# Kernel tuning notes

Hardware: AMD Instinct MI355X
Metric: run time of the kernel (lower is better)

## Reference

```python
import jax, jax.numpy as jnp
import numpy as np

# --- obs layout constants (from source) ---
OBS_TERM_DIMS = (3, 3, 3, 3, 29, 29, 29, 96)
HISTORY_LEN = 5
BASE_LIN_VEL_DIM = 3
_OFFS = [0]
for d in OBS_TERM_DIMS[:-1]:
    _OFFS.append(_OFFS[-1] + d * HISTORY_LEN)

N = 131072

def _extract_frame(x, frame_idx):
    # proprio frame: 7 terms, 99 dims total
    parts = []
    for t in range(7):
        d = OBS_TERM_DIMS[t]
        s = _OFFS[t] + frame_idx * d
        parts.append(x[:, s:s + d])
    return jnp.concatenate(parts, axis=-1)

def _extract_elevation(x):
    s = _OFFS[7] + (HISTORY_LEN - 1) * OBS_TERM_DIMS[7]
    return x[:, s:s + OBS_TERM_DIMS[7]]  # [N,96]

def setup_inputs() -> dict:
    key = jax.random.key(0)
    ks = jax.random.split(key, 16)
    s = 0.05
    return {
        "x": jax.random.normal(ks[0], (N, 975), jnp.float32),
        "vae_W1": jax.random.normal(ks[1], (480, 256), jnp.float32) * s,
        "vae_b1": jnp.zeros((256,), jnp.float32),
        "vae_Wz": jax.random.normal(ks[2], (256, 32), jnp.float32) * s,
        "vae_bz": jnp.zeros((32,), jnp.float32),
        "vae_Wv": jax.random.normal(ks[3], (256, 3), jnp.float32) * s,
        "vae_bv": jnp.zeros((3,), jnp.float32),
        "ae_W1": jax.random.normal(ks[4], (96, 64), jnp.float32) * s,
        "ae_b1": jnp.zeros((64,), jnp.float32),
        "ae_W2": jax.random.normal(ks[5], (64, 32), jnp.float32) * s,
        "ae_b2": jnp.zeros((32,), jnp.float32),
        "gate_W1": jax.random.normal(ks[6], (32, 64), jnp.float32) * s,
        "gate_b1": jnp.zeros((64,), jnp.float32),
        "gate_W2": jax.random.normal(ks[7], (64, 5), jnp.float32) * s,
        "gate_b2": jnp.zeros((5,), jnp.float32),
        "eW1": jax.random.normal(ks[8], (5, 166, 128), jnp.float32) * s,
        "eb1": jnp.zeros((5, 128), jnp.float32),
        "eW2": jax.random.normal(ks[9], (5, 128, 128), jnp.float32) * s,
        "eb2": jnp.zeros((5, 128), jnp.float32),
        "eW3": jax.random.normal(ks[10], (5, 128, 29), jnp.float32) * s,
        "eb3": jnp.zeros((5, 29), jnp.float32),
    }

def reference(x, vae_W1, vae_b1, vae_Wz, vae_bz, vae_Wv, vae_bv,
              ae_W1, ae_b1, ae_W2, ae_b2,
              gate_W1, gate_b1, gate_W2, gate_b2,
              eW1, eb1, eW2, eb2, eW3, eb3):
    elu = jax.nn.elu
    # feature extraction
    o_t = _extract_frame(x, HISTORY_LEN - 1)                       # [N,99]
    frames = [_extract_frame(x, i)[:, BASE_LIN_VEL_DIM:] for i in range(HISTORY_LEN)]
    vae_hist = jnp.concatenate(frames, axis=-1)                    # [N,480]
    e_t = _extract_elevation(x)                                    # [N,96]
    # VAE estimator (no_grad in original)
    h = elu(vae_hist @ vae_W1 + vae_b1)
    z_H = jax.lax.stop_gradient(h @ vae_Wz + vae_bz)               # [N,32]
    v_pred = jax.lax.stop_gradient(h @ vae_Wv + vae_bv)            # [N,3]
    # AE estimator (no_grad)
    ha = elu(e_t @ ae_W1 + ae_b1)
    z_E = jax.lax.stop_gradient(ha @ ae_W2 + ae_b2)                # [N,32]
    # experts: batched GEMM over 5 experts
    inp = jnp.concatenate([o_t, v_pred, z_H, z_E], axis=-1)        # [N,166]
    h1 = elu(jnp.einsum('ni,eih->neh', inp, eW1) + eb1)            # [N,5,128]
    h2 = elu(jnp.einsum('neh,ehk->nek', h1, eW2) + eb2)            # [N,5,128]
    acts = jnp.einsum('neh,ehk->nek', h2, eW3) + eb3               # [N,5,29]
    # gating
    gl = elu(z_E @ gate_W1 + gate_b1) @ gate_W2 + gate_b2          # [N,5]
    w = jax.nn.softmax(gl, axis=-1)
    return jnp.einsum('ne,nek->nk', w, acts)                       # [N,29]
```

## Files before the change

kernel.cpp:

```cpp
#include <hip/hip_runtime.h>
#include <math.h>

typedef _Float16 f16;
typedef f16  f16x8 __attribute__((ext_vector_type(8)));
typedef float f32x4 __attribute__((ext_vector_type(4)));
typedef unsigned short ushort_t;

#define MFMA16(a, b, c) __builtin_amdgcn_mfma_f32_16x16x32_f16((a), (b), (c), 0, 0, 0)

#define W1T_E 0
#define WZV_E 122880
#define A1T_E 135168
#define A2T_E 141312
#define G1T_E 143360
#define G2T_E 145408
#define E1T_E 146432
#define E2T_E 269312
#define E3T_E 351232
#define F32_B 743424

#define B0_OFF  0
#define B1_OFF  25600
#define ET_OFF  38912
#define HA_OFF  52224
#define H_OFF   38912
#define H1_OFF  38912
#define H2_OFF  56320
#define W_OFF   73728
#define MAP_OFF 75776
#define SMEM_SZ 76160

__device__ __forceinline__ float elu_f(float v) {
    float e = __expf(v) - 1.f;
    return v > 0.f ? v : e;
}

__device__ __forceinline__ unsigned pk(float a, float b) {
    ushort_t u0 = __builtin_bit_cast(ushort_t, (f16)a);
    ushort_t u1 = __builtin_bit_cast(ushort_t, (f16)b);
    return (unsigned)u0 | ((unsigned)u1 << 16);
}

__device__ __forceinline__ void store4(f16* p, f32x4 v) {
    uint2 t; t.x = pk(v[0], v[1]); t.y = pk(v[2], v[3]);
    *(uint2*)p = t;
}

__device__ __forceinline__ void elu_store4(f16* p, f32x4 v) {
    uint2 t; t.x = pk(elu_f(v[0]), elu_f(v[1])); t.y = pk(elu_f(v[2]), elu_f(v[3]));
    *(uint2*)p = t;
}

__global__ void prep_kernel(const float* __restrict__ vW1, const float* __restrict__ vWz,
                            const float* __restrict__ vWv, const float* __restrict__ aW1,
                            const float* __restrict__ aW2, const float* __restrict__ gW1,
                            const float* __restrict__ gW2, const float* __restrict__ eW1,
                            const float* __restrict__ eW2, const float* __restrict__ eW3,
                            const float* __restrict__ vbz, const float* __restrict__ vbv,
                            const float* __restrict__ eb3, const float* __restrict__ gb2,
                            char* __restrict__ ws)
{
    int i = blockIdx.x * 256 + threadIdx.x;
    f16* H = (f16*)ws;
    if (i < 122880) {
        int c = i / 480, k = i - c * 480;
        H[i] = (f16)vW1[k * 256 + c];
    } else if (i < 135168) {
        int j = i - 122880; int c = j / 256, k = j - c * 256;
        float v = (c < 32) ? vWz[k * 32 + c] : ((c < 35) ? vWv[k * 3 + (c - 32)] : 0.f);
        H[i] = (f16)v;
    } else if (i < 141312) {
        int j = i - 135168; int c = j / 96, k = j - c * 96;
        H[i] = (f16)aW1[k * 64 + c];
    } else if (i < 143360) {
        int j = i - 141312; int c = j / 64, k = j - c * 64;
        H[i] = (f16)aW2[k * 32 + c];
    } else if (i < 145408) {
        int j = i - 143360; int c = j / 32, k = j - c * 32;
        H[i] = (f16)gW1[k * 64 + c];
    } else if (i < 146432) {
        int j = i - 145408; int c = j / 64, k = j - c * 64;
        H[i] = (f16)((c < 5) ? gW2[k * 5 + c] : 0.f);
    } else if (i < 269312) {
        int j = i - 146432; int e = j / 24576, jj = j - e * 24576;
        int c = jj / 192, k = jj - c * 192;
        int ko = (k >= 5 && k < 107)   ? (k - 5)
               : (k >= 108 && k < 140) ? (k - 6)
               : (k >= 144 && k < 176) ? (k - 10) : -1;
        H[i] = (f16)((ko >= 0) ? eW1[(e * 166 + ko) * 128 + c] : 0.f);
    } else if (i < 351232) {
        int j = i - 269312; int e = j / 16384, jj = j - e * 16384;
        int c = jj / 128, k = jj - c * 128;
        H[i] = (f16)eW2[(e * 128 + k) * 128 + c];
    } else if (i < 371712) {
        int j = i - 351232; int e = j / 4096, jj = j - e * 4096;
        int c = jj / 128, k = jj - c * 128;
        H[i] = (f16)((c < 29) ? eW3[(e * 128 + k) * 29 + c] : 0.f);
    } else if (i < 371936) {
        int j = i - 371712;
        float* F = (float*)(ws + F32_B);
        float v;
        if (j < 48)       v = (j < 32) ? vbz[j] : ((j < 35) ? vbv[j - 32] : 0.f);
        else if (j < 208) { int t = j - 48; int e = t >> 5, c = t & 31;
                            v = (c < 29) ? eb3[e * 29 + c] : 0.f; }
        else              { int t = j - 208; v = (t < 5) ? gb2[t] : 0.f; }
        F[j] = v;
    }
}

__global__ __launch_bounds__(256, 2) void moe_fused(
    const float* __restrict__ x,
    const float* __restrict__ vb1,
    const float* __restrict__ ab1,
    const float* __restrict__ ab2,
    const float* __restrict__ gb1,
    const float* __restrict__ eb1,
    const float* __restrict__ eb2,
    const char* __restrict__ ws,
    float* __restrict__ out)
{
    __shared__ __align__(16) char smem[SMEM_SZ];
    const int tid  = threadIdx.x;
    const int wv   = tid >> 6;
    const int lane = tid & 63;
    const int lr   = lane & 15;
    const int lg   = lane >> 4;
    const int row0 = (int)blockIdx.x * 64;

    const f16* W1T = (const f16*)ws + W1T_E;
    const f16* WZV = (const f16*)ws + WZV_E;
    const f16* A1T = (const f16*)ws + A1T_E;
    const f16* A2T = (const f16*)ws + A2T_E;
    const f16* G1T = (const f16*)ws + G1T_E;
    const f16* G2T = (const f16*)ws + G2T_E;
    const f16* E1T = (const f16*)ws + E1T_E;
    const f16* E2T = (const f16*)ws + E2T_E;
    const f16* E3T = (const f16*)ws + E3T_E;
    const float* BZV  = (const float*)(ws + F32_B);
    const float* EB3P = BZV + 48;
    const float* GB2P = BZV + 208;

    f16* sB0 = (f16*)(smem + B0_OFF);
    f16* sB1 = (f16*)(smem + B1_OFF);
    f16* sEt = (f16*)(smem + ET_OFF);
    f16* sHA = (f16*)(smem + HA_OFF);
    f16* sH  = (f16*)(smem + H_OFF);
    f16* sH1 = (f16*)(smem + H1_OFF);
    f16* sH2 = (f16*)(smem + H2_OFF);
    float* sWf = (float*)(smem + W_OFF);
    unsigned* smap = (unsigned*)(smem + MAP_OFF);

    const char* xc = (const char*)x;
    const int srow = tid >> 2;
    const int cb   = 24 * (tid & 3);
    const bool lowc = ((tid & 3) == 0);

    if (tid < 96) {
        int c = tid; int base;
        if (c < 9)       { int t = c / 3; base = 15 + 12 * t + c; }
        else if (c < 38) base = 51 + c;
        else if (c < 67) base = 167 + c;
        else             base = 283 + c;
        smap[c] = (unsigned)(base * 4);
    }
    if (tid < 64) {
        f16* rp = sB0 + tid * 200;
        uint2 z2; z2.x = 0u; z2.y = 0u;
        *(uint2*)(rp + 0) = z2; rp[4] = (f16)0.f;
        *(uint2*)(rp + 140) = z2;
        uint4 z4; z4.x = z4.y = z4.z = z4.w = 0u;
        *(uint4*)(rp + 176) = z4; *(uint4*)(rp + 184) = z4;
    }
    if (tid < 192) {
        int r = tid / 3, c = tid - 3 * r;
        sB0[r * 200 + 5 + c] = (f16)x[(row0 + r) * 975 + 12 + c];
    }
    {
        const float* xr = x + (size_t)(row0 + srow) * 975 + 879 + cb;
        f16* dst = sEt + srow * 104 + cb;
#pragma unroll
        for (int k = 0; k < 24; k += 2) {
            *(unsigned*)(dst + k) = pk(xr[k], xr[k + 1]);
        }
    }
    __syncthreads();

    {
        f32x4 bi = *(const f32x4*)(ab1 + 16 * wv + 4 * lg);
        f32x4 acc[4];
#pragma unroll
        for (int m = 0; m < 4; ++m) acc[m] = bi;
#pragma unroll
        for (int ks = 0; ks < 3; ++ks) {
            f16x8 wf = *(const f16x8*)(A1T + (16 * wv + lr) * 96 + 32 * ks + 8 * lg);
#pragma unroll
            for (int m = 0; m < 4; ++m) {
                f16x8 bf = *(const f16x8*)(sEt + (16 * m + lr) * 104 + 32 * ks + 8 * lg);
                acc[m] = MFMA16(wf, bf, acc[m]);
            }
        }
#pragma unroll
        for (int m = 0; m < 4; ++m)
            elu_store4(sHA + (16 * m + lr) * 72 + 16 * wv + 4 * lg, acc[m]);
    }
    unsigned a_off[24];
    {
        unsigned rowb = (unsigned)(row0 + srow) * 3900u;
#pragma unroll
        for (int i = 0; i < 24; ++i) a_off[i] = rowb + smap[cb + i];
    }
    __syncthreads();

    if (wv < 2) {
        f32x4 bi = *(const f32x4*)(ab2 + 16 * wv + 4 * lg);
        f32x4 acc[4];
#pragma unroll
        for (int m = 0; m < 4; ++m) acc[m] = bi;
#pragma unroll
        for (int ks = 0; ks < 2; ++ks) {
            f16x8 wf = *(const f16x8*)(A2T + (16 * wv + lr) * 64 + 32 * ks + 8 * lg);
#pragma unroll
            for (int m = 0; m < 4; ++m) {
                f16x8 bf = *(const f16x8*)(sHA + (16 * m + lr) * 72 + 32 * ks + 8 * lg);
                acc[m] = MFMA16(wf, bf, acc[m]);
            }
        }
#pragma unroll
        for (int m = 0; m < 4; ++m)
            store4(sB0 + (16 * m + lr) * 200 + 144 + 16 * wv + 4 * lg, acc[m]);
    }
    {
        float tv[24];
#pragma unroll
        for (int i = 0; i < 24; ++i) tv[i] = *(const float*)(xc + a_off[i]);
        f16* dst = sB0 + srow * 200 + 8 + cb;
#pragma unroll
        for (int k = 0; k < 12; ++k) *(unsigned*)(dst + 2 * k) = pk(tv[2 * k], tv[2 * k + 1]);
#pragma unroll
        for (int i = 0; i < 24; ++i) a_off[i] += (lowc && i < 9) ? 12u : 116u;
    }
    __syncthreads();

    {
        f32x4 bi = *(const f32x4*)(gb1 + 16 * wv + 4 * lg);
        f32x4 acc[4];
#pragma unroll
        for (int m = 0; m < 4; ++m) acc[m] = bi;
        f16x8 wf = *(const f16x8*)(G1T + (16 * wv + lr) * 32 + 8 * lg);
#pragma unroll
        for (int m = 0; m < 4; ++m) {
            f16x8 bf = *(const f16x8*)(sB0 + (16 * m + lr) * 200 + 144 + 8 * lg);
            acc[m] = MFMA16(wf, bf, acc[m]);
        }
#pragma unroll
        for (int m = 0; m < 4; ++m)
            elu_store4(sHA + (16 * m + lr) * 72 + 16 * wv + 4 * lg, acc[m]);
    }
    __syncthreads();

    if (wv == 0) {
        f32x4 bi = *(const f32x4*)(GB2P + 4 * lg);
        f32x4 acc[4];
#pragma unroll
        for (int m = 0; m < 4; ++m) acc[m] = bi;
#pragma unroll
        for (int ks = 0; ks < 2; ++ks) {
            f16x8 wf = *(const f16x8*)(G2T + lr * 64 + 32 * ks + 8 * lg);
#pragma unroll
            for (int m = 0; m < 4; ++m) {
                f16x8 bf = *(const f16x8*)(sHA + (16 * m + lr) * 72 + 32 * ks + 8 * lg);
                acc[m] = MFMA16(wf, bf, acc[m]);
            }
        }
        if (lg == 0) {
#pragma unroll
            for (int m = 0; m < 4; ++m)
                *(f32x4*)(sWf + (16 * m + lr) * 8) = acc[m];
        } else if (lg == 1) {
#pragma unroll
            for (int m = 0; m < 4; ++m)
                sWf[(16 * m + lr) * 8 + 4] = acc[m][0];
        }
    }
    __syncthreads();

    f32x4 acc1[4][4];
#pragma unroll
    for (int nt = 0; nt < 4; ++nt) {
        f32x4 bi = *(const f32x4*)(vb1 + 64 * wv + 16 * nt + 4 * lg);
#pragma unroll
        for (int m = 0; m < 4; ++m) acc1[m][nt] = bi;
    }
    for (int f = 0; f < 5; ++f) {
        if (f == 0 && tid < 64) {
            float g[5];
#pragma unroll
            for (int e = 0; e < 5; ++e) g[e] = sWf[tid * 8 + e];
            float mx = fmaxf(fmaxf(fmaxf(g[0], g[1]), fmaxf(g[2], g[3])), g[4]);
            float s = 0.f;
#pragma unroll
            for (int e = 0; e < 5; ++e) { g[e] = __expf(g[e] - mx); s += g[e]; }
            float inv = 1.f / s;
#pragma unroll
            for (int e = 0; e < 5; ++e) sWf[tid * 8 + e] = g[e] * inv;
        }
        float tv[24];
        if (f < 4) {
#pragma unroll
            for (int i = 0; i < 24; ++i) tv[i] = *(const float*)(xc + a_off[i]);
        }
        const f16* Bp = (f & 1) ? sB1 : sB0;
        const int bst = (f & 1) ? 104 : 200;
#pragma unroll
        for (int ks = 0; ks < 3; ++ks) {
            f16x8 wf[4];
#pragma unroll
            for (int nt = 0; nt < 4; ++nt)
                wf[nt] = *(const f16x8*)(W1T + (64 * wv + 16 * nt + lr) * 480 + 96 * f + 32 * ks + 8 * lg);
#pragma unroll
            for (int m = 0; m < 4; ++m) {
                f16x8 bf = *(const f16x8*)(Bp + (16 * m + lr) * bst + 8 + 32 * ks + 8 * lg);
#pragma unroll
                for (int nt = 0; nt < 4; ++nt)
                    acc1[m][nt] = MFMA16(wf[nt], bf, acc1[m][nt]);
            }
        }
        if (f < 4) {
            f16* dst = (((f + 1) & 1) ? sB1 : sB0) + srow * (((f + 1) & 1) ? 104 : 200) + 8 + cb;
#pragma unroll
            for (int k = 0; k < 12; ++k) *(unsigned*)(dst + 2 * k) = pk(tv[2 * k], tv[2 * k + 1]);
#pragma unroll
            for (int i = 0; i < 24; ++i) a_off[i] += (lowc && i < 9) ? 12u : 116u;
        }
        if (f == 4) {
#pragma unroll
            for (int m = 0; m < 4; ++m)
#pragma unroll
                for (int nt = 0; nt < 4; ++nt)
                    elu_store4(sH + (16 * m + lr) * 264 + 64 * wv + 16 * nt + 4 * lg, acc1[m][nt]);
        }
        __syncthreads();
    }

    if (wv < 3) {
        f32x4 bz = *(const f32x4*)(BZV + 16 * wv + 4 * lg);
        f32x4 acc[4];
#pragma unroll
        for (int m = 0; m < 4; ++m) acc[m] = bz;
#pragma unroll
        for (int ks = 0; ks < 8; ++ks) {
            f16x8 wf = *(const f16x8*)(WZV + (16 * wv + lr) * 256 + 32 * ks + 8 * lg);
#pragma unroll
            for (int m = 0; m < 4; ++m) {
                f16x8 bf = *(const f16x8*)(sH + (16 * m + lr) * 264 + 32 * ks + 8 * lg);
                acc[m] = MFMA16(wf, bf, acc[m]);
            }
        }
        int j0 = 16 * wv + 4 * lg;
        if (wv < 2 || lg == 0) {
            int col = (wv < 2) ? (108 + j0) : 104;
#pragma unroll
            for (int m = 0; m < 4; ++m)
                store4(sB0 + (16 * m + lr) * 200 + col, acc[m]);
        }
    }
    __syncthreads();

    f32x4 oacc[2];
    oacc[0] = (f32x4)0.f; oacc[1] = (f32x4)0.f;

    for (int e = 0; e < 5; ++e) {
        {
            f32x4 acc[4][2];
#pragma unroll
            for (int nt = 0; nt < 2; ++nt) {
                f32x4 bi = *(const f32x4*)(eb1 + e * 128 + 32 * wv + 16 * nt + 4 * lg);
#pragma unroll
                for (int m = 0; m < 4; ++m) acc[m][nt] = bi;
            }
#pragma unroll
            for (int ks = 0; ks < 6; ++ks) {
                f16x8 wf[2];
#pragma unroll
                for (int nt = 0; nt < 2; ++nt)
                    wf[nt] = *(const f16x8*)(E1T + (e * 128 + 32 * wv + 16 * nt + lr) * 192 + 32 * ks + 8 * lg);
#pragma unroll
                for (int m = 0; m < 4; ++m) {
                    f16x8 bf = *(const f16x8*)(sB0 + (16 * m + lr) * 200 + 32 * ks + 8 * lg);
#pragma unroll
                    for (int nt = 0; nt < 2; ++nt) acc[m][nt] = MFMA16(wf[nt], bf, acc[m][nt]);
                }
            }
#pragma unroll
            for (int m = 0; m < 4; ++m)
#pragma unroll
                for (int nt = 0; nt < 2; ++nt)
                    elu_store4(sH1 + (16 * m + lr) * 136 + 32 * wv + 16 * nt + 4 * lg, acc[m][nt]);
        }
        __syncthreads();
        {
            f32x4 acc[4][2];
#pragma unroll
            for (int nt = 0; nt < 2; ++nt) {
                f32x4 bi = *(const f32x4*)(eb2 + e * 128 + 32 * wv + 16 * nt + 4 * lg);
#pragma unroll
                for (int m = 0; m < 4; ++m) acc[m][nt] = bi;
            }
#pragma unroll
            for (int ks = 0; ks < 4; ++ks) {
                f16x8 wf[2];
#pragma unroll
                for (int nt = 0; nt < 2; ++nt)
                    wf[nt] = *(const f16x8*)(E2T + (e * 128 + 32 * wv + 16 * nt + lr) * 128 + 32 * ks + 8 * lg);
#pragma unroll
                for (int m = 0; m < 4; ++m) {
                    f16x8 bf = *(const f16x8*)(sH1 + (16 * m + lr) * 136 + 32 * ks + 8 * lg);
#pragma unroll
                    for (int nt = 0; nt < 2; ++nt) acc[m][nt] = MFMA16(wf[nt], bf, acc[m][nt]);
                }
            }
#pragma unroll
            for (int m = 0; m < 4; ++m)
#pragma unroll
                for (int nt = 0; nt < 2; ++nt)
                    elu_store4(sH2 + (16 * m + lr) * 136 + 32 * wv + 16 * nt + 4 * lg, acc[m][nt]);
        }
        __syncthreads();
        {
            f32x4 acc3[2];
#pragma unroll
            for (int nt = 0; nt < 2; ++nt)
                acc3[nt] = *(const f32x4*)(EB3P + e * 32 + 16 * nt + 4 * lg);
#pragma unroll
            for (int ks = 0; ks < 4; ++ks) {
                f16x8 bf = *(const f16x8*)(sH2 + (16 * wv + lr) * 136 + 32 * ks + 8 * lg);
#pragma unroll
                for (int nt = 0; nt < 2; ++nt) {
                    f16x8 wf = *(const f16x8*)(E3T + (e * 32 + 16 * nt + lr) * 128 + 32 * ks + 8 * lg);
                    acc3[nt] = MFMA16(wf, bf, acc3[nt]);
                }
            }
            float we = sWf[(16 * wv + lr) * 8 + e];
#pragma unroll
            for (int nt = 0; nt < 2; ++nt)
#pragma unroll
                for (int r = 0; r < 4; ++r) oacc[nt][r] += we * acc3[nt][r];
        }
        __syncthreads();
    }

    {
        int row = row0 + 16 * wv + lr;
#pragma unroll
        for (int nt = 0; nt < 2; ++nt)
#pragma unroll
            for (int r = 0; r < 4; ++r) {
                int col = 16 * nt + 4 * lg + r;
                if (col < 29) out[row * 29 + col] = oacc[nt][r];
            }
    }
}

extern "C" void kernel_launch(void* const* d_in, const int* in_sizes, int n_in,
                              void* d_out, int out_size, void* d_ws, size_t ws_size,
                              hipStream_t stream)
{
    (void)n_in; (void)out_size; (void)ws_size;
    const float* x   = (const float*)d_in[0];
    const float* vW1 = (const float*)d_in[1];
    const float* vb1 = (const float*)d_in[2];
    const float* vWz = (const float*)d_in[3];
    const float* vbz = (const float*)d_in[4];
    const float* vWv = (const float*)d_in[5];
    const float* vbv = (const float*)d_in[6];
    const float* aW1 = (const float*)d_in[7];
    const float* ab1 = (const float*)d_in[8];
    const float* aW2 = (const float*)d_in[9];
    const float* ab2 = (const float*)d_in[10];
    const float* gW1 = (const float*)d_in[11];
    const float* gb1 = (const float*)d_in[12];
    const float* gW2 = (const float*)d_in[13];
    const float* gb2 = (const float*)d_in[14];
    const float* eW1 = (const float*)d_in[15];
    const float* eb1 = (const float*)d_in[16];
    const float* eW2 = (const float*)d_in[17];
    const float* eb2 = (const float*)d_in[18];
    const float* eW3 = (const float*)d_in[19];
    const float* eb3 = (const float*)d_in[20];

    int n = in_sizes[0] / 975;

    prep_kernel<<<(371936 + 255) / 256, 256, 0, stream>>>(
        vW1, vWz, vWv, aW1, aW2, gW1, gW2, eW1, eW2, eW3, vbz, vbv, eb3, gb2, (char*)d_ws);

    moe_fused<<<n / 64, 256, 0, stream>>>(
        x, vb1, ab1, ab2, gb1, eb1, eb2, (const char*)d_ws, (float*)d_out);
}
```

Baseline: 319.2 us.

## Shrink row tile to 48 and repack shared memory to fit three blocks per CU

Each block now handles 48 rows instead of 64, and the shared-memory staging buffers are overlapped so the footprint drops from about 76KB to about 47KB. Launch bounds are raised to three blocks per CU. Row loads are clamped and output stores masked so the tail block stays correct. The goal is more resident waves to hide memory and sync latency. The cost is that expert weights are reloaded per block across more blocks, MFMA reuse per weight fragment is lower, and one wave idles in the final layer.

```diff
diff --git a/kernel.cpp b/kernel.cpp
--- a/kernel.cpp
+++ b/kernel.cpp
@@ -20,15 +20,14 @@
 #define F32_B 743424
 
 #define B0_OFF  0
-#define B1_OFF  25600
-#define ET_OFF  38912
-#define HA_OFF  52224
-#define H_OFF   38912
-#define H1_OFF  38912
-#define H2_OFF  56320
-#define W_OFF   73728
-#define MAP_OFF 75776
-#define SMEM_SZ 76160
+#define SA_OFF  19200
+#define HA_OFF  29184
+#define H_OFF   19200
+#define H1_OFF  19200
+#define H2_OFF  32256
+#define W_OFF   45312
+#define MAP_OFF 46848
+#define SMEM_SZ 47232
 
 __device__ __forceinline__ float elu_f(float v) {
     float e = __expf(v) - 1.f;
@@ -108,7 +107,7 @@
     }
 }
 
-__global__ __launch_bounds__(256, 2) void moe_fused(
+__global__ __launch_bounds__(256, 3) void moe_fused(
     const float* __restrict__ x,
     const float* __restrict__ vb1,
     const float* __restrict__ ab1,
@@ -117,7 +116,8 @@
     const float* __restrict__ eb1,
     const float* __restrict__ eb2,
     const char* __restrict__ ws,
-    float* __restrict__ out)
+    float* __restrict__ out,
+    int n)
 {
     __shared__ __align__(16) char smem[SMEM_SZ];
     const int tid  = threadIdx.x;
@@ -125,7 +125,7 @@
     const int lane = tid & 63;
     const int lr   = lane & 15;
     const int lg   = lane >> 4;
-    const int row0 = (int)blockIdx.x * 64;
+    const int row0 = (int)blockIdx.x * 48;
 
     const f16* W1T = (const f16*)ws + W1T_E;
     const f16* WZV = (const f16*)ws + WZV_E;
@@ -141,8 +141,8 @@
     const float* GB2P = BZV + 208;
 
     f16* sB0 = (f16*)(smem + B0_OFF);
-    f16* sB1 = (f16*)(smem + B1_OFF);
-    f16* sEt = (f16*)(smem + ET_OFF);
+    f16* sB1 = (f16*)(smem + SA_OFF);
+    f16* sEt = (f16*)(smem + SA_OFF);
     f16* sHA = (f16*)(smem + HA_OFF);
     f16* sH  = (f16*)(smem + H_OFF);
     f16* sH1 = (f16*)(smem + H1_OFF);
@@ -154,6 +154,8 @@
     const int srow = tid >> 2;
     const int cb   = 24 * (tid & 3);
     const bool lowc = ((tid & 3) == 0);
+    const bool stg  = (tid < 192);
+    const int grow  = min(row0 + srow, n - 1);
 
     if (tid < 96) {
         int c = tid; int base;
@@ -163,7 +165,7 @@
         else             base = 283 + c;
         smap[c] = (unsigned)(base * 4);
     }
-    if (tid < 64) {
+    if (tid < 48) {
         f16* rp = sB0 + tid * 200;
         uint2 z2; z2.x = 0u; z2.y = 0u;
         *(uint2*)(rp + 0) = z2; rp[4] = (f16)0.f;
@@ -171,12 +173,13 @@
         uint4 z4; z4.x = z4.y = z4.z = z4.w = 0u;
         *(uint4*)(rp + 176) = z4; *(uint4*)(rp + 184) = z4;
     }
-    if (tid < 192) {
+    if (tid < 144) {
         int r = tid / 3, c = tid - 3 * r;
-        sB0[r * 200 + 5 + c] = (f16)x[(row0 + r) * 975 + 12 + c];
-    }
-    {
-        const float* xr = x + (size_t)(row0 + srow) * 975 + 879 + cb;
+        int gr = min(row0 + r, n - 1);
+        sB0[r * 200 + 5 + c] = (f16)x[(size_t)gr * 975 + 12 + c];
+    }
+    if (stg) {
+        const float* xr = x + (size_t)grow * 975 + 879 + cb;
         f16* dst = sEt + srow * 104 + cb;
 #pragma unroll
         for (int k = 0; k < 24; k += 2) {
@@ -187,25 +190,25 @@
 
     {
         f32x4 bi = *(const f32x4*)(ab1 + 16 * wv + 4 * lg);
-        f32x4 acc[4];
-#pragma unroll
-        for (int m = 0; m < 4; ++m) acc[m] = bi;
+        f32x4 acc[3];
+#pragma unroll
+        for (int m = 0; m < 3; ++m) acc[m] = bi;
 #pragma unroll
         for (int ks = 0; ks < 3; ++ks) {
             f16x8 wf = *(const f16x8*)(A1T + (16 * wv + lr) * 96 + 32 * ks + 8 * lg);
 #pragma unroll
-            for (int m = 0; m < 4; ++m) {
+            for (int m = 0; m < 3; ++m) {
                 f16x8 bf = *(const f16x8*)(sEt + (16 * m + lr) * 104 + 32 * ks + 8 * lg);
                 acc[m] = MFMA16(wf, bf, acc[m]);
             }
         }
 #pragma unroll
-        for (int m = 0; m < 4; ++m)
+        for (int m = 0; m < 3; ++m)
             elu_store4(sHA + (16 * m + lr) * 72 + 16 * wv + 4 * lg, acc[m]);
     }
     unsigned a_off[24];
     {
-        unsigned rowb = (unsigned)(row0 + srow) * 3900u;
+        unsigned rowb = (unsigned)grow * 3900u;
 #pragma unroll
         for (int i = 0; i < 24; ++i) a_off[i] = rowb + smap[cb + i];
     }
@@ -213,23 +216,23 @@
 
     if (wv < 2) {
         f32x4 bi = *(const f32x4*)(ab2 + 16 * wv + 4 * lg);
-        f32x4 acc[4];
-#pragma unroll
-        for (int m = 0; m < 4; ++m) acc[m] = bi;
+        f32x4 acc[3];
+#pragma unroll
+        for (int m = 0; m < 3; ++m) acc[m] = bi;
 #pragma unroll
         for (int ks = 0; ks < 2; ++ks) {
             f16x8 wf = *(const f16x8*)(A2T + (16 * wv + lr) * 64 + 32 * ks + 8 * lg);
 #pragma unroll
-            for (int m = 0; m < 4; ++m) {
+            for (int m = 0; m < 3; ++m) {
                 f16x8 bf = *(const f16x8*)(sHA + (16 * m + lr) * 72 + 32 * ks + 8 * lg);
                 acc[m] = MFMA16(wf, bf, acc[m]);
             }
         }
 #pragma unroll
-        for (int m = 0; m < 4; ++m)
+        for (int m = 0; m < 3; ++m)
             store4(sB0 + (16 * m + lr) * 200 + 144 + 16 * wv + 4 * lg, acc[m]);
     }
-    {
+    if (stg) {
         float tv[24];
 #pragma unroll
         for (int i = 0; i < 24; ++i) tv[i] = *(const float*)(xc + a_off[i]);
@@ -243,56 +246,56 @@
 
     {
         f32x4 bi = *(const f32x4*)(gb1 + 16 * wv + 4 * lg);
-        f32x4 acc[4];
-#pragma unroll
-        for (int m = 0; m < 4; ++m) acc[m] = bi;
+        f32x4 acc[3];
+#pragma unroll
+        for (int m = 0; m < 3; ++m) acc[m] = bi;
         f16x8 wf = *(const f16x8*)(G1T + (16 * wv + lr) * 32 + 8 * lg);
 #pragma unroll
-        for (int m = 0; m < 4; ++m) {
+        for (int m = 0; m < 3; ++m) {
             f16x8 bf = *(const f16x8*)(sB0 + (16 * m + lr) * 200 + 144 + 8 * lg);
             acc[m] = MFMA16(wf, bf, acc[m]);
         }
 #pragma unroll
-        for (int m = 0; m < 4; ++m)
+        for (int m = 0; m < 3; ++m)
             elu_store4(sHA + (16 * m + lr) * 72 + 16 * wv + 4 * lg, acc[m]);
     }
     __syncthreads();
 
     if (wv == 0) {
         f32x4 bi = *(const f32x4*)(GB2P + 4 * lg);
-        f32x4 acc[4];
-#pragma unroll
-        for (int m = 0; m < 4; ++m) acc[m] = bi;
+        f32x4 acc[3];
+#pragma unroll
+        for (int m = 0; m < 3; ++m) acc[m] = bi;
 #pragma unroll
         for (int ks = 0; ks < 2; ++ks) {
             f16x8 wf = *(const f16x8*)(G2T + lr * 64 + 32 * ks + 8 * lg);
 #pragma unroll
-            for (int m = 0; m < 4; ++m) {
+            for (int m = 0; m < 3; ++m) {
                 f16x8 bf = *(const f16x8*)(sHA + (16 * m + lr) * 72 + 32 * ks + 8 * lg);
                 acc[m] = MFMA16(wf, bf, acc[m]);
             }
         }
         if (lg == 0) {
 #pragma unroll
-            for (int m = 0; m < 4; ++m)
+            for (int m = 0; m < 3; ++m)
                 *(f32x4*)(sWf + (16 * m + lr) * 8) = acc[m];
         } else if (lg == 1) {
 #pragma unroll
-            for (int m = 0; m < 4; ++m)
+            for (int m = 0; m < 3; ++m)
                 sWf[(16 * m + lr) * 8 + 4] = acc[m][0];
         }
     }
     __syncthreads();
 
-    f32x4 acc1[4][4];
+    f32x4 acc1[3][4];
 #pragma unroll
     for (int nt = 0; nt < 4; ++nt) {
         f32x4 bi = *(const f32x4*)(vb1 + 64 * wv + 16 * nt + 4 * lg);
 #pragma unroll
-        for (int m = 0; m < 4; ++m) acc1[m][nt] = bi;
+        for (int m = 0; m < 3; ++m) acc1[m][nt] = bi;
     }
     for (int f = 0; f < 5; ++f) {
-        if (f == 0 && tid < 64) {
+        if (f == 0 && tid < 48) {
             float g[5];
 #pragma unroll
             for (int e = 0; e < 5; ++e) g[e] = sWf[tid * 8 + e];
@@ -305,7 +308,7 @@
             for (int e = 0; e < 5; ++e) sWf[tid * 8 + e] = g[e] * inv;
         }
         float tv[24];
-        if (f < 4) {
+        if (f < 4 && stg) {
 #pragma unroll
             for (int i = 0; i < 24; ++i) tv[i] = *(const float*)(xc + a_off[i]);
         }
@@ -318,14 +321,14 @@
             for (int nt = 0; nt < 4; ++nt)
                 wf[nt] = *(const f16x8*)(W1T + (64 * wv + 16 * nt + lr) * 480 + 96 * f + 32 * ks + 8 * lg);
 #pragma unroll
-            for (int m = 0; m < 4; ++m) {
+            for (int m = 0; m < 3; ++m) {
                 f16x8 bf = *(const f16x8*)(Bp + (16 * m + lr) * bst + 8 + 32 * ks + 8 * lg);
 #pragma unroll
                 for (int nt = 0; nt < 4; ++nt)
                     acc1[m][nt] = MFMA16(wf[nt], bf, acc1[m][nt]);
             }
         }
-        if (f < 4) {
+        if (f < 4 && stg) {
             f16* dst = (((f + 1) & 1) ? sB1 : sB0) + srow * (((f + 1) & 1) ? 104 : 200) + 8 + cb;
 #pragma unroll
             for (int k = 0; k < 12; ++k) *(unsigned*)(dst + 2 * k) = pk(tv[2 * k], tv[2 * k + 1]);
@@ -334,7 +337,7 @@
         }
         if (f == 4) {
 #pragma unroll
-            for (int m = 0; m < 4; ++m)
+            for (int m = 0; m < 3; ++m)
 #pragma unroll
                 for (int nt = 0; nt < 4; ++nt)
                     elu_store4(sH + (16 * m + lr) * 264 + 64 * wv + 16 * nt + 4 * lg, acc1[m][nt]);
@@ -344,14 +347,14 @@
 
     if (wv < 3) {
         f32x4 bz = *(const f32x4*)(BZV + 16 * wv + 4 * lg);
-        f32x4 acc[4];
-#pragma unroll
-        for (int m = 0; m < 4; ++m) acc[m] = bz;
+        f32x4 acc[3];
+#pragma unroll
+        for (int m = 0; m < 3; ++m) acc[m] = bz;
 #pragma unroll
         for (int ks = 0; ks < 8; ++ks) {
             f16x8 wf = *(const f16x8*)(WZV + (16 * wv + lr) * 256 + 32 * ks + 8 * lg);
 #pragma unroll
-            for (int m = 0; m < 4; ++m) {
+            for (int m = 0; m < 3; ++m) {
                 f16x8 bf = *(const f16x8*)(sH + (16 * m + lr) * 264 + 32 * ks + 8 * lg);
                 acc[m] = MFMA16(wf, bf, acc[m]);
             }
@@ -360,7 +363,7 @@
         if (wv < 2 || lg == 0) {
             int col = (wv < 2) ? (108 + j0) : 104;
 #pragma unroll
-            for (int m = 0; m < 4; ++m)
+            for (int m = 0; m < 3; ++m)
                 store4(sB0 + (16 * m + lr) * 200 + col, acc[m]);
         }
     }
@@ -371,12 +374,12 @@
 
     for (int e = 0; e < 5; ++e) {
         {
-            f32x4 acc[4][2];
+            f32x4 acc[3][2];
 #pragma unroll
             for (int nt = 0; nt < 2; ++nt) {
                 f32x4 bi = *(const f32x4*)(eb1 + e * 128 + 32 * wv + 16 * nt + 4 * lg);
 #pragma unroll
-                for (int m = 0; m < 4; ++m) acc[m][nt] = bi;
+                for (int m = 0; m < 3; ++m) acc[m][nt] = bi;
             }
 #pragma unroll
             for (int ks = 0; ks < 6; ++ks) {
@@ -385,26 +388,26 @@
                 for (int nt = 0; nt < 2; ++nt)
                     wf[nt] = *(const f16x8*)(E1T + (e * 128 + 32 * wv + 16 * nt + lr) * 192 + 32 * ks + 8 * lg);
 #pragma unroll
-                for (int m = 0; m < 4; ++m) {
+                for (int m = 0; m < 3; ++m) {
                     f16x8 bf = *(const f16x8*)(sB0 + (16 * m + lr) * 200 + 32 * ks + 8 * lg);
 #pragma unroll
                     for (int nt = 0; nt < 2; ++nt) acc[m][nt] = MFMA16(wf[nt], bf, acc[m][nt]);
                 }
             }
 #pragma unroll
-            for (int m = 0; m < 4; ++m)
+            for (int m = 0; m < 3; ++m)
 #pragma unroll
                 for (int nt = 0; nt < 2; ++nt)
                     elu_store4(sH1 + (16 * m + lr) * 136 + 32 * wv + 16 * nt + 4 * lg, acc[m][nt]);
         }
         __syncthreads();
         {
-            f32x4 acc[4][2];
+            f32x4 acc[3][2];
 #pragma unroll
             for (int nt = 0; nt < 2; ++nt) {
                 f32x4 bi = *(const f32x4*)(eb2 + e * 128 + 32 * wv + 16 * nt + 4 * lg);
 #pragma unroll
-                for (int m = 0; m < 4; ++m) acc[m][nt] = bi;
+                for (int m = 0; m < 3; ++m) acc[m][nt] = bi;
             }
 #pragma unroll
             for (int ks = 0; ks < 4; ++ks) {
@@ -413,20 +416,20 @@
                 for (int nt = 0; nt < 2; ++nt)
                     wf[nt] = *(const f16x8*)(E2T + (e * 128 + 32 * wv + 16 * nt + lr) * 128 + 32 * ks + 8 * lg);
 #pragma unroll
-                for (int m = 0; m < 4; ++m) {
+                for (int m = 0; m < 3; ++m) {
                     f16x8 bf = *(const f16x8*)(sH1 + (16 * m + lr) * 136 + 32 * ks + 8 * lg);
 #pragma unroll
                     for (int nt = 0; nt < 2; ++nt) acc[m][nt] = MFMA16(wf[nt], bf, acc[m][nt]);
                 }
             }
 #pragma unroll
-            for (int m = 0; m < 4; ++m)
+            for (int m = 0; m < 3; ++m)
 #pragma unroll
                 for (int nt = 0; nt < 2; ++nt)
                     elu_store4(sH2 + (16 * m + lr) * 136 + 32 * wv + 16 * nt + 4 * lg, acc[m][nt]);
         }
         __syncthreads();
-        {
+        if (wv < 3) {
             f32x4 acc3[2];
 #pragma unroll
             for (int nt = 0; nt < 2; ++nt)
@@ -449,15 +452,17 @@
         __syncthreads();
     }
 
-    {
+    if (wv < 3) {
         int row = row0 + 16 * wv + lr;
-#pragma unroll
-        for (int nt = 0; nt < 2; ++nt)
-#pragma unroll
-            for (int r = 0; r < 4; ++r) {
-                int col = 16 * nt + 4 * lg + r;
-                if (col < 29) out[row * 29 + col] = oacc[nt][r];
-            }
+        if (row < n) {
+#pragma unroll
+            for (int nt = 0; nt < 2; ++nt)
+#pragma unroll
+                for (int r = 0; r < 4; ++r) {
+                    int col = 16 * nt + 4 * lg + r;
+                    if (col < 29) out[(size_t)row * 29 + col] = oacc[nt][r];
+                }
+        }
     }
 }
 
@@ -493,6 +498,6 @@
     prep_kernel<<<(371936 + 255) / 256, 256, 0, stream>>>(
         vW1, vWz, vWv, aW1, aW2, gW1, gW2, eW1, eW2, eW3, vbz, vbv, eb3, gb2, (char*)d_ws);
 
-    moe_fused<<<n / 64, 256, 0, stream>>>(
-        x, vb1, ab1, ab2, gb1, eb1, eb2, (const char*)d_ws, (float*)d_out);
-}
+    moe_fused<<<(n + 47) / 48, 256, 0, stream>>>(
+        x, vb1, ab1, ab2, gb1, eb1, eb2, (const char*)d_ws, (float*)d_out, n);
+}
```

After: 348.0 us. 1.09x slower.

## Stage contiguous x slice in LDS and fold history gather into padded W1

Applied to the files above, without the earlier changes.

Instead of gathering the 480 scattered VAE history columns from x with per-thread offset tables across five pipelined frames, each block now copies the contiguous x columns 12..495 into shared memory with coalesced loads. The gather is moved into the prep kernel, which scatters vW1 rows into a 512-wide padded K layout, so the first GEMM runs as one 16-step K loop over the staged slice. The o_t features are then picked from that same staged buffer. This trades the reduced number of scattered global loads for about 6% extra MFMA work on the padded K, a larger shared-memory footprint, and a row-at-a-time staging loop per wave that has no double buffering.

```diff
diff --git a/kernel.cpp b/kernel.cpp
--- a/kernel.cpp
+++ b/kernel.cpp
@@ -9,26 +9,24 @@
 #define MFMA16(a, b, c) __builtin_amdgcn_mfma_f32_16x16x32_f16((a), (b), (c), 0, 0, 0)
 
 #define W1T_E 0
-#define WZV_E 122880
-#define A1T_E 135168
-#define A2T_E 141312
-#define G1T_E 143360
-#define G2T_E 145408
-#define E1T_E 146432
-#define E2T_E 269312
-#define E3T_E 351232
-#define F32_B 743424
-
-#define B0_OFF  0
-#define B1_OFF  25600
-#define ET_OFF  38912
-#define HA_OFF  52224
-#define H_OFF   38912
-#define H1_OFF  38912
-#define H2_OFF  56320
-#define W_OFF   73728
-#define MAP_OFF 75776
-#define SMEM_SZ 76160
+#define WZV_E 131072
+#define A1T_E 143360
+#define A2T_E 149504
+#define G1T_E 151552
+#define G2T_E 153600
+#define E1T_E 154624
+#define E2T_E 277504
+#define E3T_E 359424
+#define F32_B 759808
+
+#define S2_OFF   0
+#define B0_OFF   36864
+#define H2_OFF   17408
+#define ELEV_OFF 62528
+#define HA_OFF   62528
+#define ZE_OFF   71744
+#define WF_OFF   75840
+#define SMEM_SZ  77888
 
 __device__ __forceinline__ float elu_f(float v) {
     float e = __expf(v) - 1.f;
@@ -62,42 +60,55 @@
 {
     int i = blockIdx.x * 256 + threadIdx.x;
     f16* H = (f16*)ws;
-    if (i < 122880) {
-        int c = i / 480, k = i - c * 480;
-        H[i] = (f16)vW1[k * 256 + c];
-    } else if (i < 135168) {
-        int j = i - 122880; int c = j / 256, k = j - c * 256;
+    if (i < 131072) {
+        int c = i >> 9, ks = i & 511;
+        int xcol = 12 + ks;
+        float v = 0.f;
+        if (xcol >= 15 && xcol <= 494) {
+            int hc;
+            if (xcol < 60) {
+                int t = xcol / 15; int rm = xcol - 15 * t; int f = rm / 3;
+                hc = 96 * f + 3 * (t - 1) + (rm - 3 * f);
+            } else {
+                int t2 = (xcol - 60) / 145; int rm = xcol - 60 - 145 * t2; int f = rm / 29;
+                hc = 96 * f + 9 + 29 * t2 + (rm - 29 * f);
+            }
+            v = vW1[hc * 256 + c];
+        }
+        H[i] = (f16)v;
+    } else if (i < 143360) {
+        int j = i - 131072; int c = j / 256, k = j - c * 256;
         float v = (c < 32) ? vWz[k * 32 + c] : ((c < 35) ? vWv[k * 3 + (c - 32)] : 0.f);
         H[i] = (f16)v;
-    } else if (i < 141312) {
-        int j = i - 135168; int c = j / 96, k = j - c * 96;
+    } else if (i < 149504) {
+        int j = i - 143360; int c = j / 96, k = j - c * 96;
         H[i] = (f16)aW1[k * 64 + c];
-    } else if (i < 143360) {
-        int j = i - 141312; int c = j / 64, k = j - c * 64;
+    } else if (i < 151552) {
+        int j = i - 149504; int c = j / 64, k = j - c * 64;
         H[i] = (f16)aW2[k * 32 + c];
-    } else if (i < 145408) {
-        int j = i - 143360; int c = j / 32, k = j - c * 32;
+    } else if (i < 153600) {
+        int j = i - 151552; int c = j / 32, k = j - c * 32;
         H[i] = (f16)gW1[k * 64 + c];
-    } else if (i < 146432) {
-        int j = i - 145408; int c = j / 64, k = j - c * 64;
+    } else if (i < 154624) {
+        int j = i - 153600; int c = j / 64, k = j - c * 64;
         H[i] = (f16)((c < 5) ? gW2[k * 5 + c] : 0.f);
-    } else if (i < 269312) {
-        int j = i - 146432; int e = j / 24576, jj = j - e * 24576;
+    } else if (i < 277504) {
+        int j = i - 154624; int e = j / 24576, jj = j - e * 24576;
         int c = jj / 192, k = jj - c * 192;
         int ko = (k >= 5 && k < 107)   ? (k - 5)
                : (k >= 108 && k < 140) ? (k - 6)
                : (k >= 144 && k < 176) ? (k - 10) : -1;
         H[i] = (f16)((ko >= 0) ? eW1[(e * 166 + ko) * 128 + c] : 0.f);
-    } else if (i < 351232) {
-        int j = i - 269312; int e = j / 16384, jj = j - e * 16384;
+    } else if (i < 359424) {
+        int j = i - 277504; int e = j / 16384, jj = j - e * 16384;
         int c = jj / 128, k = jj - c * 128;
         H[i] = (f16)eW2[(e * 128 + k) * 128 + c];
-    } else if (i < 371712) {
-        int j = i - 351232; int e = j / 4096, jj = j - e * 4096;
+    } else if (i < 379904) {
+        int j = i - 359424; int e = j / 4096, jj = j - e * 4096;
         int c = jj / 128, k = jj - c * 128;
         H[i] = (f16)((c < 29) ? eW3[(e * 128 + k) * 29 + c] : 0.f);
-    } else if (i < 371936) {
-        int j = i - 371712;
+    } else if (i < 380128) {
+        int j = i - 379904;
         float* F = (float*)(ws + F32_B);
         float v;
         if (j < 48)       v = (j < 32) ? vbz[j] : ((j < 35) ? vbv[j - 32] : 0.f);
@@ -140,75 +151,59 @@
     const float* EB3P = BZV + 48;
     const float* GB2P = BZV + 208;
 
+    f16* sS2 = (f16*)(smem + S2_OFF);
+    f16* sEl = (f16*)(smem + ELEV_OFF);
+    f16* sHA = (f16*)(smem + HA_OFF);
+    f16* sZE = (f16*)(smem + ZE_OFF);
+    f16* sH  = (f16*)(smem + S2_OFF);
     f16* sB0 = (f16*)(smem + B0_OFF);
-    f16* sB1 = (f16*)(smem + B1_OFF);
-    f16* sEt = (f16*)(smem + ET_OFF);
-    f16* sHA = (f16*)(smem + HA_OFF);
-    f16* sH  = (f16*)(smem + H_OFF);
-    f16* sH1 = (f16*)(smem + H1_OFF);
+    f16* sH1 = (f16*)(smem + S2_OFF);
     f16* sH2 = (f16*)(smem + H2_OFF);
-    float* sWf = (float*)(smem + W_OFF);
-    unsigned* smap = (unsigned*)(smem + MAP_OFF);
-
-    const char* xc = (const char*)x;
-    const int srow = tid >> 2;
-    const int cb   = 24 * (tid & 3);
-    const bool lowc = ((tid & 3) == 0);
-
-    if (tid < 96) {
-        int c = tid; int base;
-        if (c < 9)       { int t = c / 3; base = 15 + 12 * t + c; }
-        else if (c < 38) base = 51 + c;
-        else if (c < 67) base = 167 + c;
-        else             base = 283 + c;
-        smap[c] = (unsigned)(base * 4);
-    }
-    if (tid < 64) {
-        f16* rp = sB0 + tid * 200;
-        uint2 z2; z2.x = 0u; z2.y = 0u;
-        *(uint2*)(rp + 0) = z2; rp[4] = (f16)0.f;
-        *(uint2*)(rp + 140) = z2;
-        uint4 z4; z4.x = z4.y = z4.z = z4.w = 0u;
-        *(uint4*)(rp + 176) = z4; *(uint4*)(rp + 184) = z4;
-    }
-    if (tid < 192) {
-        int r = tid / 3, c = tid - 3 * r;
-        sB0[r * 200 + 5 + c] = (f16)x[(row0 + r) * 975 + 12 + c];
-    }
+    float* sWf = (float*)(smem + WF_OFF);
+
     {
-        const float* xr = x + (size_t)(row0 + srow) * 975 + 879 + cb;
-        f16* dst = sEt + srow * 104 + cb;
-#pragma unroll
-        for (int k = 0; k < 24; k += 2) {
-            *(unsigned*)(dst + k) = pk(xr[k], xr[k + 1]);
-        }
-    }
-    __syncthreads();
-
+        if (tid < 16) *(unsigned*)(smem + 62464 + 4 * tid) = 0u;
+        const int sr0 = wv * 16;
+        for (int rr = 0; rr < 16; ++rr) {
+            const int r = sr0 + rr;
+            const float* xr = x + (size_t)(row0 + r) * 975;
+            if (lane < 48) {
+                float a = xr[879 + 2 * lane], b = xr[880 + 2 * lane];
+                *(unsigned*)(sEl + r * 104 + 2 * lane) = pk(a, b);
+            }
+            f16* dst = sS2 + r * 488;
+#pragma unroll
+            for (int j = 0; j < 4; ++j) {
+                int p = j * 64 + lane;
+                if (p < 244) {
+                    float a = 0.f, b = 0.f;
+                    if (p < 242) { a = xr[12 + 2 * p]; b = xr[13 + 2 * p]; }
+                    *(unsigned*)(dst + 2 * p) = pk(a, b);
+                }
+            }
+        }
+    }
+    __syncthreads();
+
+    f32x4 g3acc[4];
     {
         f32x4 bi = *(const f32x4*)(ab1 + 16 * wv + 4 * lg);
-        f32x4 acc[4];
-#pragma unroll
-        for (int m = 0; m < 4; ++m) acc[m] = bi;
+#pragma unroll
+        for (int m = 0; m < 4; ++m) g3acc[m] = bi;
 #pragma unroll
         for (int ks = 0; ks < 3; ++ks) {
             f16x8 wf = *(const f16x8*)(A1T + (16 * wv + lr) * 96 + 32 * ks + 8 * lg);
 #pragma unroll
             for (int m = 0; m < 4; ++m) {
-                f16x8 bf = *(const f16x8*)(sEt + (16 * m + lr) * 104 + 32 * ks + 8 * lg);
-                acc[m] = MFMA16(wf, bf, acc[m]);
-            }
-        }
-#pragma unroll
-        for (int m = 0; m < 4; ++m)
-            elu_store4(sHA + (16 * m + lr) * 72 + 16 * wv + 4 * lg, acc[m]);
-    }
-    unsigned a_off[24];
-    {
-        unsigned rowb = (unsigned)(row0 + srow) * 3900u;
-#pragma unroll
-        for (int i = 0; i < 24; ++i) a_off[i] = rowb + smap[cb + i];
-    }
+                f16x8 bf = *(const f16x8*)(sEl + (16 * m + lr) * 104 + 32 * ks + 8 * lg);
+                g3acc[m] = MFMA16(wf, bf, g3acc[m]);
+            }
+        }
+    }
+    __syncthreads();
+#pragma unroll
+    for (int m = 0; m < 4; ++m)
+        elu_store4(sHA + (16 * m + lr) * 72 + 16 * wv + 4 * lg, g3acc[m]);
     __syncthreads();
 
     if (wv < 2) {
@@ -227,17 +222,7 @@
         }
 #pragma unroll
         for (int m = 0; m < 4; ++m)
-            store4(sB0 + (16 * m + lr) * 200 + 144 + 16 * wv + 4 * lg, acc[m]);
-    }
-    {
-        float tv[24];
-#pragma unroll
-        for (int i = 0; i < 24; ++i) tv[i] = *(const float*)(xc + a_off[i]);
-        f16* dst = sB0 + srow * 200 + 8 + cb;
-#pragma unroll
-        for (int k = 0; k < 12; ++k) *(unsigned*)(dst + 2 * k) = pk(tv[2 * k], tv[2 * k + 1]);
-#pragma unroll
-        for (int i = 0; i < 24; ++i) a_off[i] += (lowc && i < 9) ? 12u : 116u;
+            store4(sZE + (16 * m + lr) * 32 + 16 * wv + 4 * lg, acc[m]);
     }
     __syncthreads();
 
@@ -249,7 +234,7 @@
         f16x8 wf = *(const f16x8*)(G1T + (16 * wv + lr) * 32 + 8 * lg);
 #pragma unroll
         for (int m = 0; m < 4; ++m) {
-            f16x8 bf = *(const f16x8*)(sB0 + (16 * m + lr) * 200 + 144 + 8 * lg);
+            f16x8 bf = *(const f16x8*)(sZE + (16 * m + lr) * 32 + 8 * lg);
             acc[m] = MFMA16(wf, bf, acc[m]);
         }
 #pragma unroll
@@ -284,6 +269,19 @@
     }
     __syncthreads();
 
+    if (tid < 64) {
+        float g[5];
+#pragma unroll
+        for (int e = 0; e < 5; ++e) g[e] = sWf[tid * 8 + e];
+        float mx = fmaxf(fmaxf(fmaxf(g[0], g[1]), fmaxf(g[2], g[3])), g[4]);
+        float s = 0.f;
+#pragma unroll
+        for (int e = 0; e < 5; ++e) { g[e] = __expf(g[e] - mx); s += g[e]; }
+        float inv = 1.f / s;
+#pragma unroll
+        for (int e = 0; e < 5; ++e) sWf[tid * 8 + e] = g[e] * inv;
+    }
+
     f32x4 acc1[4][4];
 #pragma unroll
     for (int nt = 0; nt < 4; ++nt) {
@@ -291,56 +289,62 @@
 #pragma unroll
         for (int m = 0; m < 4; ++m) acc1[m][nt] = bi;
     }
-    for (int f = 0; f < 5; ++f) {
-        if (f == 0 && tid < 64) {
-            float g[5];
-#pragma unroll
-            for (int e = 0; e < 5; ++e) g[e] = sWf[tid * 8 + e];
-            float mx = fmaxf(fmaxf(fmaxf(g[0], g[1]), fmaxf(g[2], g[3])), g[4]);
-            float s = 0.f;
-#pragma unroll
-            for (int e = 0; e < 5; ++e) { g[e] = __expf(g[e] - mx); s += g[e]; }
-            float inv = 1.f / s;
-#pragma unroll
-            for (int e = 0; e < 5; ++e) sWf[tid * 8 + e] = g[e] * inv;
-        }
-        float tv[24];
-        if (f < 4) {
-#pragma unroll
-            for (int i = 0; i < 24; ++i) tv[i] = *(const float*)(xc + a_off[i]);
-        }
-        const f16* Bp = (f & 1) ? sB1 : sB0;
-        const int bst = (f & 1) ? 104 : 200;
-#pragma unroll
-        for (int ks = 0; ks < 3; ++ks) {
-            f16x8 wf[4];
+#pragma unroll
+    for (int ks = 0; ks < 16; ++ks) {
+        f16x8 wf[4];
+#pragma unroll
+        for (int nt = 0; nt < 4; ++nt)
+            wf[nt] = *(const f16x8*)(W1T + (64 * wv + 16 * nt + lr) * 512 + 32 * ks + 8 * lg);
+#pragma unroll
+        for (int m = 0; m < 4; ++m) {
+            f16x8 bf = *(const f16x8*)(sS2 + (16 * m + lr) * 488 + 32 * ks + 8 * lg);
 #pragma unroll
             for (int nt = 0; nt < 4; ++nt)
-                wf[nt] = *(const f16x8*)(W1T + (64 * wv + 16 * nt + lr) * 480 + 96 * f + 32 * ks + 8 * lg);
-#pragma unroll
-            for (int m = 0; m < 4; ++m) {
-                f16x8 bf = *(const f16x8*)(Bp + (16 * m + lr) * bst + 8 + 32 * ks + 8 * lg);
-#pragma unroll
-                for (int nt = 0; nt < 4; ++nt)
-                    acc1[m][nt] = MFMA16(wf[nt], bf, acc1[m][nt]);
-            }
-        }
-        if (f < 4) {
-            f16* dst = (((f + 1) & 1) ? sB1 : sB0) + srow * (((f + 1) & 1) ? 104 : 200) + 8 + cb;
-#pragma unroll
-            for (int k = 0; k < 12; ++k) *(unsigned*)(dst + 2 * k) = pk(tv[2 * k], tv[2 * k + 1]);
-#pragma unroll
-            for (int i = 0; i < 24; ++i) a_off[i] += (lowc && i < 9) ? 12u : 116u;
-        }
-        if (f == 4) {
-#pragma unroll
-            for (int m = 0; m < 4; ++m)
-#pragma unroll
-                for (int nt = 0; nt < 4; ++nt)
-                    elu_store4(sH + (16 * m + lr) * 264 + 64 * wv + 16 * nt + 4 * lg, acc1[m][nt]);
-        }
-        __syncthreads();
-    }
+                acc1[m][nt] = MFMA16(wf[nt], bf, acc1[m][nt]);
+        }
+    }
+    const int r_ot = tid >> 2, sub = tid & 3;
+    ushort_t otv[25];
+#pragma unroll
+    for (int i = 0; i < 25; ++i) {
+        int j = sub + 4 * i;
+        if (j < 99) {
+            int s;
+            if (j < 3) s = j;
+            else if (j < 12) { int jj = j - 3; int t = jj / 3;
+                               s = 15 * (t + 1) + (jj - 3 * t); }
+            else { int jj = j - 12; int t2 = jj / 29;
+                   s = 164 + 145 * t2 + (jj - 29 * t2); }
+            otv[i] = __builtin_bit_cast(ushort_t, sS2[r_ot * 488 + s]);
+        }
+    }
+    __syncthreads();
+
+#pragma unroll
+    for (int m = 0; m < 4; ++m)
+#pragma unroll
+        for (int nt = 0; nt < 4; ++nt)
+            elu_store4(sH + (16 * m + lr) * 264 + 64 * wv + 16 * nt + 4 * lg, acc1[m][nt]);
+#pragma unroll
+    for (int i = 0; i < 25; ++i) {
+        int j = sub + 4 * i;
+        if (j < 99) sB0[r_ot * 200 + 5 + j] = __builtin_bit_cast(f16, otv[i]);
+    }
+    {
+        char* b0r = (char*)sB0 + r_ot * 400;
+        if (sub == 0) { *(uint2*)(b0r + 0) = (uint2){0u, 0u}; *(ushort_t*)(b0r + 8) = 0; }
+        else if (sub == 1) { *(uint2*)(b0r + 280) = (uint2){0u, 0u}; }
+        else if (sub == 2) { *(uint4*)(b0r + 352) = (uint4){0u,0u,0u,0u}; }
+        else               { *(uint4*)(b0r + 368) = (uint4){0u,0u,0u,0u}; }
+    }
+#pragma unroll
+    for (int it = 0; it < 2; ++it) {
+        int idx = tid + 256 * it;
+        int r = idx >> 3, c4 = idx & 7;
+        uint2 v = *(uint2*)((char*)sZE + r * 64 + 8 * c4);
+        *(uint2*)((char*)sB0 + r * 400 + 288 + 8 * c4) = v;
+    }
+    __syncthreads();
 
     if (wv < 3) {
         f32x4 bz = *(const f32x4*)(BZV + 16 * wv + 4 * lg);
@@ -456,7 +460,7 @@
 #pragma unroll
             for (int r = 0; r < 4; ++r) {
                 int col = 16 * nt + 4 * lg + r;
-                if (col < 29) out[row * 29 + col] = oacc[nt][r];
+                if (col < 29) out[(size_t)row * 29 + col] = oacc[nt][r];
             }
     }
 }
@@ -490,7 +494,7 @@
 
     int n = in_sizes[0] / 975;
 
-    prep_kernel<<<(371936 + 255) / 256, 256, 0, stream>>>(
+    prep_kernel<<<(380128 + 255) / 256, 256, 0, stream>>>(
         vW1, vWz, vWv, aW1, aW2, gW1, gW2, eW1, eW2, eW3, vbz, vbv, eb3, gb2, (char*)d_ws);
 
     moe_fused<<<n / 64, 256, 0, stream>>>(
```

New measurement: 329.9 us. 1.03x slower.
